# Kernel optimization log

Measured on AMD Instinct MI355X. Metric: run time of the kernel, lower is better.

The kernel has to match this reference:

```python
import jax, jax.numpy as jnp
import numpy as np

N_NODES = 50000
N_EDGES = 800000
IN_FEAT = 100
OUT_FEAT = 100
NUM_RELS = 200
NUM_HEADS = 3
NUM_BASES = 100
SUB_IN = 1   # in_feat // num_bases
SUB_OUT = 1  # out_feat // num_bases


def setup_inputs() -> dict:
    key = jax.random.key(0)
    ks = jax.random.split(key, 10)
    return {
        "h": jax.random.normal(ks[0], (N_NODES, IN_FEAT), jnp.float32),
        "e": jax.random.normal(ks[1], (N_EDGES, IN_FEAT), jnp.float32),
        "norm": jax.random.uniform(ks[2], (N_NODES, 1), jnp.float32),
        "weight": jax.random.normal(ks[3], (NUM_RELS, NUM_BASES * SUB_IN * SUB_OUT), jnp.float32) * 0.1,
        "attn": jax.random.normal(ks[4], (NUM_RELS, NUM_HEADS, OUT_FEAT), jnp.float32) * 0.1,
        "fc_w": jax.random.normal(ks[5], (IN_FEAT, OUT_FEAT * NUM_HEADS), jnp.float32) * 0.1,
        "loop_w": jax.random.normal(ks[6], (IN_FEAT, OUT_FEAT), jnp.float32) * 0.1,
        "rel": jax.random.randint(ks[7], (N_EDGES,), 0, NUM_RELS, jnp.int32),
        "src": jax.random.randint(ks[8], (N_EDGES,), 0, N_NODES, jnp.int32),
        "dst": jax.random.randint(ks[9], (N_EDGES,), 0, N_NODES, jnp.int32),
    }


def reference(h, e, norm, weight, attn, fc_w, loop_w, rel, src, dst):
    E = rel.shape[0]
    # --- relation-indexed block-diagonal message (torch.bmm over blocks) ---
    W_e = weight[rel].reshape(E, NUM_BASES, SUB_IN, SUB_OUT)        # per-edge block weights
    h_src = h[src].reshape(E, NUM_BASES, SUB_IN)                    # gathered src features
    msg = jnp.einsum('ebi,ebio->ebo', h_src, W_e).reshape(E, OUT_FEAT)
    # --- edge-feature attention fuse ---
    a_e = attn[rel]                                                 # (E, H, OUT)
    fc_e = (e @ fc_w).reshape(E, NUM_HEADS, OUT_FEAT)               # fc(edge)
    feat = jax.nn.leaky_relu(a_e * fc_e, 0.2).sum(axis=1)           # (E, OUT)
    msg = msg + feat
    # --- scatter-sum aggregation to dst nodes, then norm + self-loop ---
    agg = jax.ops.segment_sum(msg, dst, num_segments=N_NODES)       # (N, OUT)
    node = agg * norm
    loop_message = h @ loop_w
    return node + loop_message
```

## Files before the change

kernel.cpp:

```cpp
#include <hip/hip_runtime.h>
#include <hip/hip_bf16.h>

#define N_NODES 50000
#define N_EDGES 800000
#define IN_FEAT 100
#define OUT_FEAT 100
#define NUM_RELS 200
#define NUM_HEADS 3

#define KP 128
#define NPH 112
#define MB  128
#define NT_O 7
#define WPB 8
#define MSGW 100
#define BROWS 312
#define HSTRIDE 25600

#define WS_B       0u
#define WS_LW      86016u
#define WS_CNT     114688u
#define WS_OFFS    315392u
#define WS_CURSOR  516096u
#define WS_BSUM    716800u
#define WS_SLOT    717056u
#define WS_MSG     7117056u
#define WS_NEEDED  167117056u
#define NNODES_PAD 50176

typedef __attribute__((ext_vector_type(8))) short short8;
typedef __attribute__((ext_vector_type(4))) float f32x4;

__device__ __forceinline__ unsigned short f2bf(float f) {
    unsigned u = __builtin_bit_cast(unsigned, f);
    unsigned r = u + 0x7FFFu + ((u >> 16) & 1u);
    return (unsigned short)(r >> 16);
}
__device__ __forceinline__ float bf2f(unsigned hs) {
    return __builtin_bit_cast(float, hs << 16);
}

__global__ __launch_bounds__(256) void build_B(const float* __restrict__ fc_w,
                                               unsigned short* __restrict__ Bws) {
    int idx = blockIdx.x * 256 + threadIdx.x;
    if (idx >= BROWS * 16) return;
    int n = idx >> 4, g = idx & 15;
    int head = n / 100, nl = n - head * 100;
    int kt = g >> 2, g4 = g & 3;
    unsigned p[4] = {0u, 0u, 0u, 0u};
    if (n < 300) {
#pragma unroll
        for (int half = 0; half < 2; ++half) {
#pragma unroll
            for (int jp = 0; jp < 2; ++jp) {
                int k_lo = kt * 32 + half * 16 + g4 * 4 + jp * 2;
                int k_hi = k_lo + 1;
                float vlo = (k_lo < IN_FEAT)
                          ? fc_w[k_lo * (OUT_FEAT * NUM_HEADS) + head * OUT_FEAT + nl] : 0.f;
                float vhi = (k_hi < IN_FEAT)
                          ? fc_w[k_hi * (OUT_FEAT * NUM_HEADS) + head * OUT_FEAT + nl] : 0.f;
                p[half * 2 + jp] = (unsigned)f2bf(vlo) | ((unsigned)f2bf(vhi) << 16);
            }
        }
    }
    unsigned off = (unsigned)(n * 256) + (((unsigned)(g * 16)) ^ (((unsigned)(nl & 7)) << 4));
    *reinterpret_cast<int4*>(reinterpret_cast<char*>(Bws) + off) =
        make_int4((int)p[0], (int)p[1], (int)p[2], (int)p[3]);
}

__global__ __launch_bounds__(256) void build_LW(const float* __restrict__ loop_w,
                                                unsigned short* __restrict__ LWws) {
    int idx = blockIdx.x * 256 + threadIdx.x;
    if (idx >= NPH * 16) return;
    int nl = idx >> 4, g = idx & 15;
    int kt = g >> 2, g4 = g & 3;
    unsigned p[4];
#pragma unroll
    for (int half = 0; half < 2; ++half) {
#pragma unroll
        for (int jp = 0; jp < 2; ++jp) {
            int k_lo = kt * 32 + half * 16 + g4 * 4 + jp * 2;
            int k_hi = k_lo + 1;
            float vlo = (k_lo < IN_FEAT && nl < OUT_FEAT) ? loop_w[k_lo * OUT_FEAT + nl] : 0.f;
            float vhi = (k_hi < IN_FEAT && nl < OUT_FEAT) ? loop_w[k_hi * OUT_FEAT + nl] : 0.f;
            p[half * 2 + jp] = (unsigned)f2bf(vlo) | ((unsigned)f2bf(vhi) << 16);
        }
    }
    reinterpret_cast<int4*>(LWws)[idx] = make_int4((int)p[0], (int)p[1], (int)p[2], (int)p[3]);
}

__global__ __launch_bounds__(512, 2) void loop_gemm(const float* __restrict__ h,
                                                    const unsigned short* __restrict__ LWimg,
                                                    float* __restrict__ out) {
    const int tid = threadIdx.x;
    const int wave = tid >> 6, lane = tid & 63;
    const int lrow = lane & 15, lk = lane >> 4;
    const int rbase = blockIdx.x * MB;
    const int grow = rbase + wave * 16 + lrow;
    const bool ok = grow < N_NODES;
    const float* ap = h + (size_t)grow * IN_FEAT;

    short8 afrag[4];
#pragma unroll
    for (int kt = 0; kt < 4; ++kt) {
        int k0 = kt * 32 + lk * 4, k1 = k0 + 16;
        float4 va = (ok && k0 + 4 <= IN_FEAT) ? *reinterpret_cast<const float4*>(ap + k0)
                                              : make_float4(0.f, 0.f, 0.f, 0.f);
        float4 vb = (ok && k1 + 4 <= IN_FEAT) ? *reinterpret_cast<const float4*>(ap + k1)
                                              : make_float4(0.f, 0.f, 0.f, 0.f);
        afrag[kt][0] = (short)f2bf(va.x); afrag[kt][1] = (short)f2bf(va.y);
        afrag[kt][2] = (short)f2bf(va.z); afrag[kt][3] = (short)f2bf(va.w);
        afrag[kt][4] = (short)f2bf(vb.x); afrag[kt][5] = (short)f2bf(vb.y);
        afrag[kt][6] = (short)f2bf(vb.z); afrag[kt][7] = (short)f2bf(vb.w);
    }

#pragma unroll
    for (int nt = 0; nt < NT_O; ++nt) {
        f32x4 acc = (f32x4){0.f, 0.f, 0.f, 0.f};
#pragma unroll
        for (int kt = 0; kt < 4; ++kt) {
            short8 bfrag = *reinterpret_cast<const short8*>(
                LWimg + ((nt * 16 + lrow) * KP + kt * 32 + lk * 8));
            acc = __builtin_amdgcn_mfma_f32_16x16x32_bf16(afrag[kt], bfrag, acc, 0, 0, 0);
        }
        int o = nt * 16 + lrow;
        if (o < OUT_FEAT) {
#pragma unroll
            for (int r = 0; r < 4; ++r) {
                int crow = rbase + wave * 16 + lk * 4 + r;
                if (crow < N_NODES) out[(size_t)crow * OUT_FEAT + o] = acc[r];
            }
        }
    }
}

__global__ __launch_bounds__(512) void hist_kernel(const int* __restrict__ dst,
                                                   int* __restrict__ cnt) {
    int e = blockIdx.x * 512 + threadIdx.x;
    if (e < N_EDGES) atomicAdd(&cnt[dst[e]], 1);
}

__global__ __launch_bounds__(1024) void scan1(const int* __restrict__ cnt,
                                              int* __restrict__ offs,
                                              int* __restrict__ bsum) {
    __shared__ int s[1024];
    int i = blockIdx.x * 1024 + threadIdx.x;
    int v = (i < N_NODES) ? cnt[i] : 0;
    s[threadIdx.x] = v;
    __syncthreads();
    for (int d = 1; d < 1024; d <<= 1) {
        int t = (threadIdx.x >= d) ? s[threadIdx.x - d] : 0;
        __syncthreads();
        s[threadIdx.x] += t;
        __syncthreads();
    }
    offs[i] = s[threadIdx.x] - v;
    if (threadIdx.x == 1023) bsum[blockIdx.x] = s[1023];
}

__global__ __launch_bounds__(64) void scan2(int* __restrict__ bsum) {
    __shared__ int s[64];
    int v = (threadIdx.x < NNODES_PAD / 1024) ? bsum[threadIdx.x] : 0;
    s[threadIdx.x] = v;
    __syncthreads();
    for (int d = 1; d < 64; d <<= 1) {
        int t = (threadIdx.x >= d) ? s[threadIdx.x - d] : 0;
        __syncthreads();
        s[threadIdx.x] += t;
        __syncthreads();
    }
    bsum[threadIdx.x] = s[threadIdx.x] - v;
}

__global__ __launch_bounds__(1024) void scan3(int* __restrict__ offs,
                                              const int* __restrict__ bsum,
                                              int* __restrict__ cursor) {
    int i = blockIdx.x * 1024 + threadIdx.x;
    int v = offs[i] + bsum[blockIdx.x];
    offs[i] = v;
    cursor[i] = v;
}

__global__ __launch_bounds__(512) void scatter_kernel(const int* __restrict__ dst,
                                                      int* __restrict__ cursor,
                                                      int* __restrict__ slotmap) {
    int e = blockIdx.x * 512 + threadIdx.x;
    if (e < N_EDGES) {
        int p = atomicAdd(&cursor[dst[e]], 1);
        slotmap[e] = p;
    }
}

template<bool TOWS>
__global__ __launch_bounds__(512, 2) void feat_kernel(
        const float* __restrict__ efeat, const int* __restrict__ rel,
        const unsigned short* __restrict__ Bimg, const float* __restrict__ attn,
        const float* __restrict__ h, const float* __restrict__ weight,
        const float* __restrict__ norm, const int* __restrict__ src,
        const int* __restrict__ dst, const int* __restrict__ slotmap,
        float* __restrict__ out, unsigned short* __restrict__ msgws,
        int ntiles) {

    __shared__ __align__(16) unsigned short Blds[BROWS * 128];

    const int tid = threadIdx.x;
    {
        const int4* sp = reinterpret_cast<const int4*>(Bimg);
        int4* dp = reinterpret_cast<int4*>(Blds);
        for (int i = tid; i < BROWS * 128 / 8; i += 512) dp[i] = sp[i];
    }
    __syncthreads();

    const int wave = tid >> 6, lane = tid & 63;
    const int lrow = lane & 15, lk = lane >> 4;
    const int gstride = gridDim.x * WPB;
    int tile = blockIdx.x * WPB + wave;
    if (tile >= ntiles) return;

    const char* Bc = reinterpret_cast<const char*>(Blds);
    int bkt[4];
#pragma unroll
    for (int kt = 0; kt < 4; ++kt)
        bkt[kt] = lrow * 256 + ((kt * 64 + lk * 16) ^ ((lrow & 7) << 4));

    float4 pa[8];
    int prl[4], psr[4], pdd[4];

    auto prefetch = [&](int t) {
        int eb = t * 16;
        const float* ap = efeat + (size_t)(eb + lrow) * IN_FEAT;
#pragma unroll
        for (int kt = 0; kt < 4; ++kt) {
            int k0 = kt * 32 + lk * 4, k1 = k0 + 16;
            pa[kt * 2]     = (k0 + 4 <= IN_FEAT) ? *reinterpret_cast<const float4*>(ap + k0)
                                                 : make_float4(0.f, 0.f, 0.f, 0.f);
            pa[kt * 2 + 1] = (k1 + 4 <= IN_FEAT) ? *reinterpret_cast<const float4*>(ap + k1)
                                                 : make_float4(0.f, 0.f, 0.f, 0.f);
        }
        const int* rp = rel + eb + lk * 4;
        const int* sp = src + eb + lk * 4;
        const int* dp = dst + eb + lk * 4;
#pragma unroll
        for (int r = 0; r < 4; ++r) { prl[r] = rp[r]; psr[r] = sp[r]; pdd[r] = dp[r]; }
    };

    prefetch(tile);

    while (true) {
        const int cur = tile;
        const int tb = cur * 16;

        short8 afrag[4];
#pragma unroll
        for (int kt = 0; kt < 4; ++kt) {
            float4 va = pa[kt * 2], vb = pa[kt * 2 + 1];
            afrag[kt][0] = (short)f2bf(va.x); afrag[kt][1] = (short)f2bf(va.y);
            afrag[kt][2] = (short)f2bf(va.z); afrag[kt][3] = (short)f2bf(va.w);
            afrag[kt][4] = (short)f2bf(vb.x); afrag[kt][5] = (short)f2bf(vb.y);
            afrag[kt][6] = (short)f2bf(vb.z); afrag[kt][7] = (short)f2bf(vb.w);
        }
        int aoff[4], hoff[4], woff[4];
        float nm[4];
#pragma unroll
        for (int r = 0; r < 4; ++r) {
            aoff[r] = prl[r] * (NUM_HEADS * OUT_FEAT);
            woff[r] = prl[r] * OUT_FEAT;
            hoff[r] = psr[r] * IN_FEAT;
            nm[r]   = norm[pdd[r]];
        }
        int slot_r[4], dd_r[4];
        if (TOWS) {
#pragma unroll
            for (int r = 0; r < 4; ++r) slot_r[r] = slotmap[tb + lk * 4 + r];
        } else {
#pragma unroll
            for (int r = 0; r < 4; ++r) dd_r[r] = pdd[r];
        }

        int next = tile + gstride;
        bool more = next < ntiles;
        prefetch(more ? next : cur);

        float feat[NT_O][4];
#pragma unroll
        for (int nt = 0; nt < NT_O; ++nt) {
            int o = nt * 16 + lrow;
#pragma unroll
            for (int r = 0; r < 4; ++r)
                feat[nt][r] = (o < OUT_FEAT) ? h[hoff[r] + o] * weight[woff[r] + o] : 0.f;
        }

#pragma unroll 1
        for (int hh = 0; hh < NUM_HEADS; ++hh) {
            const char* Bh = Bc + hh * HSTRIDE;
#pragma unroll
            for (int nt = 0; nt < NT_O; ++nt) {
                f32x4 acc = (f32x4){0.f, 0.f, 0.f, 0.f};
#pragma unroll
                for (int kt = 0; kt < 4; ++kt) {
                    short8 bfrag = *reinterpret_cast<const short8*>(
                        Bh + bkt[kt] + nt * 4096);
                    acc = __builtin_amdgcn_mfma_f32_16x16x32_bf16(afrag[kt], bfrag, acc, 0, 0, 0);
                }
                int o = nt * 16 + lrow;
                if (o < OUT_FEAT) {
                    int oo = hh * OUT_FEAT + o;
#pragma unroll
                    for (int r = 0; r < 4; ++r) {
                        float v = acc[r] * attn[aoff[r] + oo];
                        feat[nt][r] += (v > 0.f) ? v : 0.2f * v;
                    }
                }
            }
        }

        if (TOWS) {
#pragma unroll
            for (int nt = 0; nt < NT_O; ++nt) {
                int o = nt * 16 + lrow;
                if (o < OUT_FEAT) {
#pragma unroll
                    for (int r = 0; r < 4; ++r)
                        msgws[(size_t)slot_r[r] * MSGW + o] = f2bf(feat[nt][r] * nm[r]);
                }
            }
        } else {
#pragma unroll
            for (int nt = 0; nt < NT_O; ++nt) {
                int o = nt * 16 + lrow;
                if (o < OUT_FEAT) {
#pragma unroll
                    for (int r = 0; r < 4; ++r)
                        atomicAdd(&out[(size_t)dd_r[r] * OUT_FEAT + o],
                                  feat[nt][r] * nm[r]);
                }
            }
        }

        if (!more) break;
        tile = next;
    }
}

__global__ __launch_bounds__(256, 4) void agg_kernel(
        const unsigned short* __restrict__ msgws, const int* __restrict__ offs,
        const int* __restrict__ cnt, float* __restrict__ out) {
    int wv = threadIdx.x >> 6, lane = threadIdx.x & 63;
    int n = blockIdx.x * 4 + wv;
    if (n >= N_NODES) return;
    int start = offs[n], deg = cnt[n];
    if (deg == 0 || lane >= OUT_FEAT / 2) return;
    const unsigned* mp = reinterpret_cast<const unsigned*>(msgws);
    float ax = 0.f, ay = 0.f;
    int k = start, end = start + deg;
    for (; k + 4 <= end; k += 4) {
        unsigned u0 = mp[(size_t)k * (MSGW / 2) + lane];
        unsigned u1 = mp[(size_t)(k + 1) * (MSGW / 2) + lane];
        unsigned u2 = mp[(size_t)(k + 2) * (MSGW / 2) + lane];
        unsigned u3 = mp[(size_t)(k + 3) * (MSGW / 2) + lane];
        ax += bf2f(u0 & 0xffffu) + bf2f(u1 & 0xffffu) + bf2f(u2 & 0xffffu) + bf2f(u3 & 0xffffu);
        ay += bf2f(u0 >> 16) + bf2f(u1 >> 16) + bf2f(u2 >> 16) + bf2f(u3 >> 16);
    }
    for (; k < end; ++k) {
        unsigned u0 = mp[(size_t)k * (MSGW / 2) + lane];
        ax += bf2f(u0 & 0xffffu);
        ay += bf2f(u0 >> 16);
    }
    float2* op = reinterpret_cast<float2*>(out + (size_t)n * OUT_FEAT) + lane;
    float2 curv = *op;
    curv.x += ax; curv.y += ay;
    *op = curv;
}

extern "C" void kernel_launch(void* const* d_in, const int* in_sizes, int n_in,
                              void* d_out, int out_size, void* d_ws, size_t ws_size,
                              hipStream_t stream) {
    const float* h      = (const float*)d_in[0];
    const float* efeat  = (const float*)d_in[1];
    const float* norm   = (const float*)d_in[2];
    const float* weight = (const float*)d_in[3];
    const float* attn   = (const float*)d_in[4];
    const float* fc_w   = (const float*)d_in[5];
    const float* loop_w = (const float*)d_in[6];
    const int*   rel    = (const int*)d_in[7];
    const int*   src    = (const int*)d_in[8];
    const int*   dst    = (const int*)d_in[9];
    float* out = (float*)d_out;

    char* ws = (char*)d_ws;
    unsigned short* Bimg  = (unsigned short*)(ws + WS_B);
    unsigned short* LWimg = (unsigned short*)(ws + WS_LW);
    int* cnt     = (int*)(ws + WS_CNT);
    int* offs    = (int*)(ws + WS_OFFS);
    int* cursor  = (int*)(ws + WS_CURSOR);
    int* bsum    = (int*)(ws + WS_BSUM);
    int* slotmap = (int*)(ws + WS_SLOT);
    unsigned short* msgws = (unsigned short*)(ws + WS_MSG);

    build_B<<<(BROWS * 16 + 255) / 256, 256, 0, stream>>>(fc_w, Bimg);
    build_LW<<<(NPH * 16 + 255) / 256, 256, 0, stream>>>(loop_w, LWimg);
    loop_gemm<<<(N_NODES + MB - 1) / MB, 512, 0, stream>>>(h, LWimg, out);

    const int ntiles = N_EDGES / 16;

    if (ws_size >= (size_t)WS_NEEDED) {
        hipMemsetAsync(cnt, 0, NNODES_PAD * sizeof(int), stream);
        hist_kernel<<<(N_EDGES + 511) / 512, 512, 0, stream>>>(dst, cnt);
        scan1<<<NNODES_PAD / 1024, 1024, 0, stream>>>(cnt, offs, bsum);
        scan2<<<1, 64, 0, stream>>>(bsum);
        scan3<<<NNODES_PAD / 1024, 1024, 0, stream>>>(offs, bsum, cursor);
        scatter_kernel<<<(N_EDGES + 511) / 512, 512, 0, stream>>>(dst, cursor, slotmap);

        feat_kernel<true><<<512, 512, 0, stream>>>(
            efeat, rel, Bimg, attn, h, weight, norm, src, dst, slotmap,
            out, msgws, ntiles);
        agg_kernel<<<(N_NODES + 3) / 4, 256, 0, stream>>>(msgws, offs, cnt, out);
    } else {
        feat_kernel<false><<<512, 512, 0, stream>>>(
            efeat, rel, Bimg, attn, h, weight, norm, src, dst, nullptr,
            out, msgws, ntiles);
    }
}
```

Measured before the change: 401.8 us.

## Drop software prefetch in feat kernel and use 6-wave blocks for occupancy

```diff
diff --git a/kernel.cpp b/kernel.cpp
--- a/kernel.cpp
+++ b/kernel.cpp
@@ -12,7 +12,7 @@
 #define NPH 112
 #define MB  128
 #define NT_O 7
-#define WPB 8
+#define WPB 6
 #define MSGW 100
 #define BROWS 312
 #define HSTRIDE 25600
@@ -192,7 +192,7 @@
 }
 
 template<bool TOWS>
-__global__ __launch_bounds__(512, 2) void feat_kernel(
+__global__ __launch_bounds__(384, 3) void feat_kernel(
         const float* __restrict__ efeat, const int* __restrict__ rel,
         const unsigned short* __restrict__ Bimg, const float* __restrict__ attn,
         const float* __restrict__ h, const float* __restrict__ weight,
@@ -207,7 +207,7 @@
     {
         const int4* sp = reinterpret_cast<const int4*>(Bimg);
         int4* dp = reinterpret_cast<int4*>(Blds);
-        for (int i = tid; i < BROWS * 128 / 8; i += 512) dp[i] = sp[i];
+        for (int i = tid; i < BROWS * 128 / 8; i += 384) dp[i] = sp[i];
     }
     __syncthreads();
 
@@ -215,7 +215,6 @@
     const int lrow = lane & 15, lk = lane >> 4;
     const int gstride = gridDim.x * WPB;
     int tile = blockIdx.x * WPB + wave;
-    if (tile >= ntiles) return;
 
     const char* Bc = reinterpret_cast<const char*>(Blds);
     int bkt[4];
@@ -223,63 +222,38 @@
     for (int kt = 0; kt < 4; ++kt)
         bkt[kt] = lrow * 256 + ((kt * 64 + lk * 16) ^ ((lrow & 7) << 4));
 
-    float4 pa[8];
-    int prl[4], psr[4], pdd[4];
-
-    auto prefetch = [&](int t) {
-        int eb = t * 16;
-        const float* ap = efeat + (size_t)(eb + lrow) * IN_FEAT;
-#pragma unroll
-        for (int kt = 0; kt < 4; ++kt) {
-            int k0 = kt * 32 + lk * 4, k1 = k0 + 16;
-            pa[kt * 2]     = (k0 + 4 <= IN_FEAT) ? *reinterpret_cast<const float4*>(ap + k0)
-                                                 : make_float4(0.f, 0.f, 0.f, 0.f);
-            pa[kt * 2 + 1] = (k1 + 4 <= IN_FEAT) ? *reinterpret_cast<const float4*>(ap + k1)
-                                                 : make_float4(0.f, 0.f, 0.f, 0.f);
-        }
-        const int* rp = rel + eb + lk * 4;
-        const int* sp = src + eb + lk * 4;
-        const int* dp = dst + eb + lk * 4;
-#pragma unroll
-        for (int r = 0; r < 4; ++r) { prl[r] = rp[r]; psr[r] = sp[r]; pdd[r] = dp[r]; }
-    };
-
-    prefetch(tile);
-
-    while (true) {
-        const int cur = tile;
-        const int tb = cur * 16;
+    while (tile < ntiles) {
+        const int tb = tile * 16;
 
         short8 afrag[4];
-#pragma unroll
-        for (int kt = 0; kt < 4; ++kt) {
-            float4 va = pa[kt * 2], vb = pa[kt * 2 + 1];
-            afrag[kt][0] = (short)f2bf(va.x); afrag[kt][1] = (short)f2bf(va.y);
-            afrag[kt][2] = (short)f2bf(va.z); afrag[kt][3] = (short)f2bf(va.w);
-            afrag[kt][4] = (short)f2bf(vb.x); afrag[kt][5] = (short)f2bf(vb.y);
-            afrag[kt][6] = (short)f2bf(vb.z); afrag[kt][7] = (short)f2bf(vb.w);
-        }
-        int aoff[4], hoff[4], woff[4];
+        {
+            const float* ap = efeat + (size_t)(tb + lrow) * IN_FEAT;
+#pragma unroll
+            for (int kt = 0; kt < 4; ++kt) {
+                int k0 = kt * 32 + lk * 4, k1 = k0 + 16;
+                float4 va = (k0 + 4 <= IN_FEAT) ? *reinterpret_cast<const float4*>(ap + k0)
+                                                : make_float4(0.f, 0.f, 0.f, 0.f);
+                float4 vb = (k1 + 4 <= IN_FEAT) ? *reinterpret_cast<const float4*>(ap + k1)
+                                                : make_float4(0.f, 0.f, 0.f, 0.f);
+                afrag[kt][0] = (short)f2bf(va.x); afrag[kt][1] = (short)f2bf(va.y);
+                afrag[kt][2] = (short)f2bf(va.z); afrag[kt][3] = (short)f2bf(va.w);
+                afrag[kt][4] = (short)f2bf(vb.x); afrag[kt][5] = (short)f2bf(vb.y);
+                afrag[kt][6] = (short)f2bf(vb.z); afrag[kt][7] = (short)f2bf(vb.w);
+            }
+        }
+        int prl[4], psr[4];
         float nm[4];
+        int slot_r[4], dd_r[4];
 #pragma unroll
         for (int r = 0; r < 4; ++r) {
-            aoff[r] = prl[r] * (NUM_HEADS * OUT_FEAT);
-            woff[r] = prl[r] * OUT_FEAT;
-            hoff[r] = psr[r] * IN_FEAT;
-            nm[r]   = norm[pdd[r]];
-        }
-        int slot_r[4], dd_r[4];
-        if (TOWS) {
-#pragma unroll
-            for (int r = 0; r < 4; ++r) slot_r[r] = slotmap[tb + lk * 4 + r];
-        } else {
-#pragma unroll
-            for (int r = 0; r < 4; ++r) dd_r[r] = pdd[r];
-        }
-
-        int next = tile + gstride;
-        bool more = next < ntiles;
-        prefetch(more ? next : cur);
+            int ei = tb + lk * 4 + r;
+            prl[r] = rel[ei];
+            psr[r] = src[ei];
+            int d = dst[ei];
+            nm[r] = norm[d];
+            if (TOWS) slot_r[r] = slotmap[ei];
+            else      dd_r[r] = d;
+        }
 
         float feat[NT_O][4];
 #pragma unroll
@@ -287,7 +261,10 @@
             int o = nt * 16 + lrow;
 #pragma unroll
             for (int r = 0; r < 4; ++r)
-                feat[nt][r] = (o < OUT_FEAT) ? h[hoff[r] + o] * weight[woff[r] + o] : 0.f;
+                feat[nt][r] = (o < OUT_FEAT)
+                            ? h[(size_t)psr[r] * IN_FEAT + o] *
+                              weight[(size_t)prl[r] * OUT_FEAT + o]
+                            : 0.f;
         }
 
 #pragma unroll 1
@@ -307,7 +284,7 @@
                     int oo = hh * OUT_FEAT + o;
 #pragma unroll
                     for (int r = 0; r < 4; ++r) {
-                        float v = acc[r] * attn[aoff[r] + oo];
+                        float v = acc[r] * attn[prl[r] * (NUM_HEADS * OUT_FEAT) + oo];
                         feat[nt][r] += (v > 0.f) ? v : 0.2f * v;
                     }
                 }
@@ -337,8 +314,7 @@
             }
         }
 
-        if (!more) break;
-        tile = next;
+        tile += gstride;
     }
 }
 
@@ -411,12 +387,12 @@
         scan3<<<NNODES_PAD / 1024, 1024, 0, stream>>>(offs, bsum, cursor);
         scatter_kernel<<<(N_EDGES + 511) / 512, 512, 0, stream>>>(dst, cursor, slotmap);
 
-        feat_kernel<true><<<512, 512, 0, stream>>>(
+        feat_kernel<true><<<512, 384, 0, stream>>>(
             efeat, rel, Bimg, attn, h, weight, norm, src, dst, slotmap,
             out, msgws, ntiles);
         agg_kernel<<<(N_NODES + 3) / 4, 256, 0, stream>>>(msgws, offs, cnt, out);
     } else {
-        feat_kernel<false><<<512, 512, 0, stream>>>(
+        feat_kernel<false><<<512, 384, 0, stream>>>(
             efeat, rel, Bimg, attn, h, weight, norm, src, dst, nullptr,
             out, msgws, ntiles);
     }
```

Result: slower. 422.4 us (+5.1%).
